# Optimization experiments

Measured on AMD Instinct MI355X. Metric: run time of the kernel, lower is better.

Reference implementation:

```python
import jax, jax.numpy as jnp
import numpy as np

T, B, NMUL = 730, 1000, 8
NEARZERO = 1e-5
LENF = 15
A_LO, A_HI = 0.1, 1.0
B_LO, B_HI = 50.0, 500.0
C_LO, C_HI = 0.0, 1.0
D_LO, D_HI = 0.01, 0.9
RA_LO, RA_HI = 0.0, 2.9
RB_LO, RB_HI = 0.0, 6.5
S_INIT, G_INIT = 50.0, 10.0


def setup_inputs() -> dict:
    key = jax.random.key(0)
    k1, k2 = jax.random.split(key)
    # forcing: prcp in [0,10) mm/day, pet in [0,5) mm/day
    x = jax.random.uniform(k1, (T, B, 2), dtype=jnp.float32) * jnp.array([10.0, 5.0], dtype=jnp.float32)
    # NN-produced raw params in [0,1): 4*NMUL physical + 2 routing
    raw_phy_static = jax.random.uniform(k2, (B, 4 * NMUL + 2), dtype=jnp.float32)
    return {"x": x, "raw_phy_static": raw_phy_static}


def _descale(p, lo, hi):
    return p * (hi - lo) + lo


def _uh_gamma(rout_a, rout_b):
    # gamma-distribution unit hydrograph, (B,) params -> (B, LENF) kernel
    aa = jax.nn.relu(rout_a)[:, None] + 0.1      # shape parameter
    theta = jax.nn.relu(rout_b)[:, None] + 0.5   # scale parameter
    t = jnp.arange(0.5, LENF, 1.0, dtype=jnp.float32)[None, :]  # midpoints 0.5..14.5
    logw = (aa - 1.0) * jnp.log(t) - t / theta - jax.scipy.special.gammaln(aa) - aa * jnp.log(theta)
    w = jnp.exp(logw)
    return w / w.sum(1, keepdims=True)


def _uh_conv(q, UH):
    # causal per-basin convolution: y[b,t] = sum_k q[b,t-k]*UH[b,k]; q (B,T), UH (B,LENF)
    n = q.shape[1]
    conv1 = lambda qb, wb: jnp.convolve(qb, wb, mode='full')[:n]
    return jax.vmap(conv1)(q, UH)


def reference(x, raw_phy_static):
    phy = raw_phy_static[:, :4 * NMUL].reshape(B, 4, NMUL)  # (B,4,NMUL)
    a = _descale(phy[:, 0], A_LO, A_HI)
    b = _descale(phy[:, 1], B_LO, B_HI)
    c = _descale(phy[:, 2], C_LO, C_HI)
    d = _descale(phy[:, 3], D_LO, D_HI)
    rout_a = _descale(raw_phy_static[:, 4 * NMUL], RA_LO, RA_HI)  # (B,)
    rout_b = _descale(raw_phy_static[:, 4 * NMUL + 1], RB_LO, RB_HI)

    ones_mul = jnp.ones((1, 1, NMUL), dtype=x.dtype)
    P = x[:, :, 0:1] * ones_mul    # (T,B,NMUL)
    PET = x[:, :, 1:2] * ones_mul  # (T,B,NMUL)

    S0 = jnp.full((B, NMUL), S_INIT, dtype=x.dtype)
    G0 = jnp.full((B, NMUL), G_INIT, dtype=x.dtype)

    def step(carry, inp):
        S, G = carry
        p, pet = inp
        W = p + S                                   # available water
        term = (W + b) / (2.0 * a)
        Y = term - jnp.sqrt(jnp.maximum(term * term - W * b / a, NEARZERO))  # ET opportunity
        S_new = Y * jnp.exp(-pet / b)               # soil storage
        AET = Y - S_new                             # actual ET
        avail = W - Y                               # water available for runoff/recharge
        Qsurf = (1.0 - c) * avail                   # direct runoff
        G_new = (G + c * avail) / (1.0 + d)         # groundwater storage
        Qgw = d * G_new                             # baseflow
        Qsim = Qsurf + Qgw
        return (S_new, G_new), (Qsim, Qsurf, Qgw, AET, S_new, G_new, W, Y)

    (_, _), (Qsim, Qsurf, Qgw, AET, Sout, Gout, Wout, Yout) = jax.lax.scan(step, (S0, G0), (P, PET))

    UH = _uh_gamma(rout_a, rout_b)                  # (B,LENF)
    Qs = _uh_conv(Qsim.mean(-1).T, UH).T[..., None]        # routed streamflow (T,B,1)
    Qsurf_r = _uh_conv(Qsurf.mean(-1).T, UH).T[..., None]  # routed surface runoff
    Qgw_r = _uh_conv(Qgw.mean(-1).T, UH).T[..., None]      # routed groundwater flow

    out = jnp.concatenate([
        Qs, Qsurf_r, Qgw_r,
        AET.mean(-1, keepdims=True),
        Sout.mean(-1, keepdims=True),
        Gout.mean(-1, keepdims=True),
    ], axis=-1)  # (T,B,6)
    return out
```

## Files before the change

kernel.cpp:

```cpp
#include <hip/hip_runtime.h>
#include <math.h>

#define T_STEPS 730
#define NB      1000
#define LENF    15
#define NEARZ   1e-5f
#define TPAD    736
#define NLANES  8000

#define STEPA(CURV, Q, SIDX)                                                   \
  {                                                                            \
    float pcp = (CURV).x, pet = (CURV).y;                                      \
    float W     = pcp + S;                                                     \
    float term  = fmaf(W, inv2a, pb2a);                                        \
    float disc  = fmaf(term, term, -(W * boa));                                \
    float r     = __builtin_amdgcn_sqrtf(fmaxf(disc, NEARZ));                  \
    float Y     = term - r;                                                    \
    float e     = __builtin_amdgcn_exp2f(pet * ninvbl2);                       \
    float Sn    = Y * e;                                                       \
    float avail = W - Y;                                                       \
    float Gn    = fmaf(pc, avail, G) * inv1pd;                                 \
    S = Sn; G = Gn;                                                            \
    sr[(Q)] = Sn;                                                              \
    gr[(Q)] = Gn;                                                              \
    if (((Q) & 3) == 3) {                                                      \
      *(float4*)(pS + (SIDX) - 3) =                                            \
          make_float4(sr[(Q) - 3], sr[(Q) - 2], sr[(Q) - 1], sr[(Q)]);         \
      *(float4*)(pG + (SIDX) - 3) =                                            \
          make_float4(gr[(Q) - 3], gr[(Q) - 2], gr[(Q) - 1], gr[(Q)]);         \
    }                                                                          \
  }

#define PREFETCH(BUF, CI)                                                      \
  _Pragma("unroll")                                                            \
  for (int j = 0; j < 8; ++j) {                                                \
      int tt = (CI) * 8 + j;                                                   \
      tt = tt < T_STEPS ? tt : (T_STEPS - 1);                                  \
      BUF[j] = xf[tt * NB + b];                                                \
  }                                                                            \
  __builtin_amdgcn_sched_barrier(0);

__global__ __launch_bounds__(64, 1) void scan_state(const float* __restrict__ x,
                                                    const float* __restrict__ raw,
                                                    float* __restrict__ snp,
                                                    float* __restrict__ gnp) {
    const int L   = threadIdx.x;
    const int gid = blockIdx.x * 64 + L;
    const int b   = gid >> 3;
    const int m   = gid & 7;

    const float* rp = raw + b * 34;
    float pa = rp[0 * 8 + m] * 0.9f + 0.1f;
    float pb = rp[1 * 8 + m] * 450.0f + 50.0f;
    float pc = rp[2 * 8 + m];
    float pd = rp[3 * 8 + m] * 0.89f + 0.01f;

    float inv2a   = 1.0f / (2.0f * pa);
    float pb2a    = pb * inv2a;
    float boa     = pb / pa;
    float ninvbl2 = -1.4426950408889634f / pb;
    float inv1pd  = 1.0f / (1.0f + pd);

    float* pS = snp + (size_t)gid * TPAD;
    float* pG = gnp + (size_t)gid * TPAD;

    float S = 50.0f, G = 10.0f;
    float sr[16], gr[16];

    const float2* __restrict__ xf = (const float2*)x;

    float2 A[8], Bb[8], Cc[8];
    PREFETCH(A, 0)
    PREFETCH(Bb, 1)

    for (int g = 0; g < 15; ++g) {
        const int c0 = 6 * g;
        PREFETCH(Cc, c0 + 2)
#pragma unroll
        for (int j = 0; j < 8; ++j) STEPA(A[j],  j,      j)
        PREFETCH(A, c0 + 3)
#pragma unroll
        for (int j = 0; j < 8; ++j) STEPA(Bb[j], 8 + j,  8 + j)
        PREFETCH(Bb, c0 + 4)
#pragma unroll
        for (int j = 0; j < 8; ++j) STEPA(Cc[j], j,      16 + j)
        PREFETCH(Cc, c0 + 5)
#pragma unroll
        for (int j = 0; j < 8; ++j) STEPA(A[j],  8 + j,  24 + j)
        PREFETCH(A, c0 + 6)
#pragma unroll
        for (int j = 0; j < 8; ++j) STEPA(Bb[j], j,      32 + j)
        PREFETCH(Bb, c0 + 7)
#pragma unroll
        for (int j = 0; j < 8; ++j) STEPA(Cc[j], 8 + j,  40 + j)
        pS += 48; pG += 48;
    }
#pragma unroll
    for (int j = 0; j < 8; ++j) STEPA(A[j], j, j)
    STEPA(Bb[0], 8, 8)
    STEPA(Bb[1], 9, 9)
    *(float2*)(pS + 8) = make_float2(sr[8], sr[9]);
    *(float2*)(pG + 8) = make_float2(gr[8], gr[9]);
}

__global__ __launch_bounds__(256) void finalize(const float* __restrict__ x,
                                                const float* __restrict__ raw,
                                                const float* __restrict__ snp,
                                                const float* __restrict__ gnp,
                                                float* __restrict__ out) {
    __shared__ float qs_sh[270], qg_sh[270];

    const int b     = blockIdx.y;
    const int tbase = blockIdx.x * 256;
    const int tid   = threadIdx.x;

    const float* rp = raw + b * 34;
    float e2s[8], omc_[8], d_[8];
#pragma unroll
    for (int m = 0; m < 8; ++m) {
        float pb = rp[8 + m] * 450.0f + 50.0f;
        e2s[m]  = 1.4426950408889634f / pb;
        omc_[m] = 1.0f - rp[16 + m];
        d_[m]   = rp[24 + m] * 0.89f + 0.01f;
    }

    const float2* __restrict__ xf = (const float2*)x;

#pragma unroll
    for (int it = 0; it < 2; ++it) {
        int idx = tid + it * 256;
        if (idx < 270) {
            int tt = tbase + idx - 14;
            float qs = 0.0f, qg = 0.0f;
            if (tt >= 0 && tt < T_STEPS) {
                float2 pc2 = xf[tt * NB + b];
                float p = pc2.x, pet = pc2.y;
                float aet = 0.0f, ssum = 0.0f, gsum = 0.0f;
                int tprev = tt > 0 ? tt - 1 : 0;
#pragma unroll
                for (int m = 0; m < 8; ++m) {
                    const float* rowS = snp + (size_t)(b * 8 + m) * TPAD;
                    const float* rowG = gnp + (size_t)(b * 8 + m) * TPAD;
                    float sn = rowS[tt];
                    float sp = tt > 0 ? rowS[tprev] : 50.0f;
                    float gn = rowG[tt];
                    float y  = sn * __builtin_amdgcn_exp2f(pet * e2s[m]);
                    float avail = (p + sp) - y;
                    qs   += omc_[m] * avail;
                    qg   += d_[m] * gn;
                    aet  += y - sn;
                    ssum += sn;
                    gsum += gn;
                }
                if (idx >= 14) {
                    float* o = out + ((size_t)tt * NB + b) * 6;
                    o[3] = aet * 0.125f;
                    o[4] = ssum * 0.125f;
                    o[5] = gsum * 0.125f;
                }
            }
            qs_sh[idx] = qs;
            qg_sh[idx] = qg;
        }
    }
    __syncthreads();

    const int t = tbase + tid;
    if (t >= T_STEPS) return;

    float ra = rp[32] * 2.9f;
    float rb = rp[33] * 6.5f;
    float aa = fmaxf(ra, 0.0f) + 0.1f;
    float th = fmaxf(rb, 0.0f) + 0.5f;
    float inv_th = 1.0f / th;
    float am1 = aa - 1.0f;
    float w[LENF];
    float sw = 0.0f;
#pragma unroll
    for (int k = 0; k < LENF; ++k) {
        float tk = (float)k + 0.5f;
        w[k] = __expf(am1 * __logf(tk) - tk * inv_th);
        sw += w[k];
    }
    float invs = 0.125f / sw;
    float ys = 0.0f, yg = 0.0f;
#pragma unroll
    for (int k = 0; k < LENF; ++k) {
        float wk = w[k] * invs;
        ys = fmaf(qs_sh[tid + 14 - k], wk, ys);
        yg = fmaf(qg_sh[tid + 14 - k], wk, yg);
    }
    float* o = out + ((size_t)t * NB + b) * 6;
    o[0] = ys + yg;
    o[1] = ys;
    o[2] = yg;
}

template <int CTRL>
__device__ __forceinline__ float dpp_mov(float x) {
    int xi = __builtin_bit_cast(int, x);
    int r  = __builtin_amdgcn_update_dpp(0, xi, CTRL, 0xF, 0xF, true);
    return __builtin_bit_cast(float, r);
}
__device__ __forceinline__ float sum8(float v) {
    v += dpp_mov<0xB1>(v);
    v += dpp_mov<0x4E>(v);
    v += dpp_mov<0x141>(v);
    return v;
}

#define STEPF(CURV)                                                            \
  {                                                                            \
    float pcp = (CURV).x, pet = (CURV).y;                                      \
    float W     = pcp + S;                                                     \
    float term  = fmaf(W, inv2a, pb2a);                                        \
    float disc  = fmaf(term, term, -(W * boa));                                \
    float r     = __builtin_amdgcn_sqrtf(fmaxf(disc, NEARZ));                  \
    float Y     = term - r;                                                    \
    float e     = __builtin_amdgcn_exp2f(pet * ninvbl2);                       \
    float Sn    = Y * e;                                                       \
    float AET   = Y - Sn;                                                      \
    float avail = W - Y;                                                       \
    float Qs    = omc * avail;                                                 \
    float Gn    = fmaf(pc, avail, G) * inv1pd;                                 \
    float Qg    = pd * Gn;                                                     \
    S = Sn; G = Gn;                                                            \
    float qs_s = sum8(Qs);                                                     \
    float qg_s = sum8(Qg);                                                     \
    float ae_s = sum8(AET);                                                    \
    float s_s  = sum8(Sn);                                                     \
    float g_s  = sum8(Gn);                                                     \
    float v = qs_s;                                                            \
    v = (m == 1) ? qg_s : v;                                                   \
    v = (m == 2) ? ae_s : v;                                                   \
    v = (m == 3) ? s_s  : v;                                                   \
    v = (m >= 4) ? g_s  : v;                                                   \
    *optr = v * 0.125f;                                                        \
    optr += incr;                                                              \
  }

__global__ __launch_bounds__(64, 1) void scan_fb(const float* __restrict__ x,
                                                 const float* __restrict__ raw,
                                                 float* __restrict__ out,
                                                 float* __restrict__ qs_ws,
                                                 float* __restrict__ qg_ws,
                                                 float* __restrict__ dummy) {
    const int L  = threadIdx.x;
    const int lb = L >> 3;
    const int m  = L & 7;
    const int b  = blockIdx.x * 8 + lb;

    const float* rp = raw + b * 34;
    float pa = rp[0 * 8 + m] * 0.9f + 0.1f;
    float pb = rp[1 * 8 + m] * 450.0f + 50.0f;
    float pc = rp[2 * 8 + m];
    float pd = rp[3 * 8 + m] * 0.89f + 0.01f;
    float inv2a   = 1.0f / (2.0f * pa);
    float pb2a    = pb * inv2a;
    float boa     = pb / pa;
    float ninvbl2 = -1.4426950408889634f / pb;
    float omc     = 1.0f - pc;
    float inv1pd  = 1.0f / (1.0f + pd);

    float* optr;
    long long incr;
    if      (m == 0) { optr = qs_ws + b;                      incr = NB;     }
    else if (m == 1) { optr = qg_ws + b;                      incr = NB;     }
    else if (m <= 4) { optr = out + (long long)b * 6 + m + 1; incr = NB * 6; }
    else             { optr = dummy + (blockIdx.x * 64 + L);  incr = 0;      }

    float S = 50.0f, G = 10.0f;
    const float2* __restrict__ xf = (const float2*)x;

    float2 A[10], B[10], C[10];
#pragma unroll
    for (int j = 0; j < 10; ++j) A[j] = xf[j * NB + b];
#pragma unroll
    for (int j = 0; j < 10; ++j) B[j] = xf[(10 + j) * NB + b];

    for (int cg = 0; cg < 24; ++cg) {
        const int c0 = 3 * cg;
#pragma unroll
        for (int j = 0; j < 10; ++j) C[j] = xf[((c0 + 2) * 10 + j) * NB + b];
        __builtin_amdgcn_sched_barrier(0);
#pragma unroll
        for (int j = 0; j < 10; ++j) STEPF(A[j]);
#pragma unroll
        for (int j = 0; j < 10; ++j) A[j] = xf[((c0 + 3) * 10 + j) * NB + b];
        __builtin_amdgcn_sched_barrier(0);
#pragma unroll
        for (int j = 0; j < 10; ++j) STEPF(B[j]);
#pragma unroll
        for (int j = 0; j < 10; ++j) {
            int t = (c0 + 4) * 10 + j;
            t = t < T_STEPS ? t : (T_STEPS - 1);
            B[j] = xf[t * NB + b];
        }
        __builtin_amdgcn_sched_barrier(0);
#pragma unroll
        for (int j = 0; j < 10; ++j) STEPF(C[j]);
    }
#pragma unroll
    for (int j = 0; j < 10; ++j) STEPF(A[j]);
}

__global__ __launch_bounds__(256) void uh_fb(const float* __restrict__ raw,
                                             float* __restrict__ uh) {
    int b = blockIdx.x * 256 + threadIdx.x;
    if (b >= NB) return;
    float ra = raw[b * 34 + 32] * 2.9f;
    float rb = raw[b * 34 + 33] * 6.5f;
    float aa = fmaxf(ra, 0.0f) + 0.1f;
    float th = fmaxf(rb, 0.0f) + 0.5f;
    float inv_th = 1.0f / th;
    float am1 = aa - 1.0f;
    float w[LENF];
    float s = 0.0f;
#pragma unroll
    for (int k = 0; k < LENF; ++k) {
        float t = (float)k + 0.5f;
        w[k] = __expf(am1 * __logf(t) - t * inv_th);
        s += w[k];
    }
    float invs = 1.0f / s;
#pragma unroll
    for (int k = 0; k < LENF; ++k) uh[k * NB + b] = w[k] * invs;
}

__global__ __launch_bounds__(256) void conv_fb(const float* __restrict__ qs_ws,
                                               const float* __restrict__ qg_ws,
                                               const float* __restrict__ uh,
                                               float* __restrict__ out) {
    int b = blockIdx.x * 256 + threadIdx.x;
    int t = blockIdx.y;
    if (b >= NB) return;
    float ys = 0.0f, yg = 0.0f;
    int kmax = t < (LENF - 1) ? t : (LENF - 1);
    for (int k = 0; k <= kmax; ++k) {
        float w = uh[k * NB + b];
        ys = fmaf(qs_ws[(t - k) * NB + b], w, ys);
        yg = fmaf(qg_ws[(t - k) * NB + b], w, yg);
    }
    float* o = out + (t * NB + b) * 6;
    o[0] = ys + yg;
    o[1] = ys;
    o[2] = yg;
}

extern "C" void kernel_launch(void* const* d_in, const int* in_sizes, int n_in,
                              void* d_out, int out_size, void* d_ws, size_t ws_size,
                              hipStream_t stream) {
    const float* x   = (const float*)d_in[0];
    const float* raw = (const float*)d_in[1];
    float* out = (float*)d_out;

    const size_t need = (size_t)NLANES * TPAD * 2 * sizeof(float);
    if (ws_size >= need) {
        float* snp = (float*)d_ws;
        float* gnp = snp + (size_t)NLANES * TPAD;
        scan_state<<<dim3(NLANES / 64), dim3(64),  0, stream>>>(x, raw, snp, gnp);
        finalize  <<<dim3(3, NB),       dim3(256), 0, stream>>>(x, raw, snp, gnp, out);
    } else {
        float* qs = (float*)d_ws;
        float* qg = qs + (size_t)T_STEPS * NB;
        float* uh = qg + (size_t)T_STEPS * NB;
        float* dm = uh + (size_t)LENF * NB;
        uh_fb  <<<dim3((NB + 255) / 256),          dim3(256), 0, stream>>>(raw, uh);
        scan_fb<<<dim3(NB / 8),                    dim3(64),  0, stream>>>(x, raw, out, qs, qg, dm);
        conv_fb<<<dim3((NB + 255) / 256, T_STEPS), dim3(256), 0, stream>>>(qs, qg, uh, out);
    }
}
```

Measured before the change: 126.7 us.

## Deepen scan prefetch to four buffers and share UH weights via LDS

The sequential scan kernel now rotates four 8-step input buffers instead of three, so loads are issued further ahead of use. Each chunk's S/G results are stored as grouped float4 writes at the start of the next chunk rather than inside the step macro. Index clamping is confined to the final prefetch. In the finalize kernel, the 15 unit-hydrograph weights are computed once per block by 15 threads and shared through LDS, instead of every thread running the log/exp per tap. This adds register pressure from the extra buffer and one more LDS read path.

```diff
diff --git a/kernel.cpp b/kernel.cpp
--- a/kernel.cpp
+++ b/kernel.cpp
@@ -8,7 +8,7 @@
 #define TPAD    736
 #define NLANES  8000
 
-#define STEPA(CURV, Q, SIDX)                                                   \
+#define STEPA(CURV, RJ)                                                        \
   {                                                                            \
     float pcp = (CURV).x, pet = (CURV).y;                                      \
     float W     = pcp + S;                                                     \
@@ -21,17 +21,16 @@
     float avail = W - Y;                                                       \
     float Gn    = fmaf(pc, avail, G) * inv1pd;                                 \
     S = Sn; G = Gn;                                                            \
-    sr[(Q)] = Sn;                                                              \
-    gr[(Q)] = Gn;                                                              \
-    if (((Q) & 3) == 3) {                                                      \
-      *(float4*)(pS + (SIDX) - 3) =                                            \
-          make_float4(sr[(Q) - 3], sr[(Q) - 2], sr[(Q) - 1], sr[(Q)]);         \
-      *(float4*)(pG + (SIDX) - 3) =                                            \
-          make_float4(gr[(Q) - 3], gr[(Q) - 2], gr[(Q) - 1], gr[(Q)]);         \
-    }                                                                          \
+    sr[(RJ)] = Sn;                                                             \
+    gr[(RJ)] = Gn;                                                             \
   }
 
-#define PREFETCH(BUF, CI)                                                      \
+#define PF(BUF, CI)                                                            \
+  _Pragma("unroll")                                                            \
+  for (int j = 0; j < 8; ++j) BUF[j] = xf[((CI) * 8 + j) * NB + b];            \
+  __builtin_amdgcn_sched_barrier(0);
+
+#define PFC(BUF, CI)                                                           \
   _Pragma("unroll")                                                            \
   for (int j = 0; j < 8; ++j) {                                                \
       int tt = (CI) * 8 + j;                                                   \
@@ -39,6 +38,18 @@
       BUF[j] = xf[tt * NB + b];                                                \
   }                                                                            \
   __builtin_amdgcn_sched_barrier(0);
+
+#define FLUSH(R)                                                               \
+  *(float4*)(pS)     = make_float4(sr[(R)], sr[(R)+1], sr[(R)+2], sr[(R)+3]);  \
+  *(float4*)(pS + 4) = make_float4(sr[(R)+4], sr[(R)+5], sr[(R)+6], sr[(R)+7]);\
+  *(float4*)(pG)     = make_float4(gr[(R)], gr[(R)+1], gr[(R)+2], gr[(R)+3]);  \
+  *(float4*)(pG + 4) = make_float4(gr[(R)+4], gr[(R)+5], gr[(R)+6], gr[(R)+7]);\
+  pS += 8; pG += 8;
+
+#define CHUNK8(RFL, BUFPF, CI, BUFC, RFILL)                                    \
+  { FLUSH(RFL) PF(BUFPF, CI) }                                                 \
+  _Pragma("unroll")                                                            \
+  for (int j = 0; j < 8; ++j) STEPA(BUFC[j], (RFILL) + j)
 
 __global__ __launch_bounds__(64, 1) void scan_state(const float* __restrict__ x,
                                                     const float* __restrict__ raw,
@@ -69,38 +80,37 @@
 
     const float2* __restrict__ xf = (const float2*)x;
 
-    float2 A[8], Bb[8], Cc[8];
-    PREFETCH(A, 0)
-    PREFETCH(Bb, 1)
-
-    for (int g = 0; g < 15; ++g) {
-        const int c0 = 6 * g;
-        PREFETCH(Cc, c0 + 2)
-#pragma unroll
-        for (int j = 0; j < 8; ++j) STEPA(A[j],  j,      j)
-        PREFETCH(A, c0 + 3)
-#pragma unroll
-        for (int j = 0; j < 8; ++j) STEPA(Bb[j], 8 + j,  8 + j)
-        PREFETCH(Bb, c0 + 4)
-#pragma unroll
-        for (int j = 0; j < 8; ++j) STEPA(Cc[j], j,      16 + j)
-        PREFETCH(Cc, c0 + 5)
-#pragma unroll
-        for (int j = 0; j < 8; ++j) STEPA(A[j],  8 + j,  24 + j)
-        PREFETCH(A, c0 + 6)
-#pragma unroll
-        for (int j = 0; j < 8; ++j) STEPA(Bb[j], j,      32 + j)
-        PREFETCH(Bb, c0 + 7)
-#pragma unroll
-        for (int j = 0; j < 8; ++j) STEPA(Cc[j], 8 + j,  40 + j)
-        pS += 48; pG += 48;
-    }
-#pragma unroll
-    for (int j = 0; j < 8; ++j) STEPA(A[j], j, j)
-    STEPA(Bb[0], 8, 8)
-    STEPA(Bb[1], 9, 9)
-    *(float2*)(pS + 8) = make_float2(sr[8], sr[9]);
-    *(float2*)(pG + 8) = make_float2(gr[8], gr[9]);
+    float2 A[8], B[8], C[8], D[8];
+    PF(A, 0) PF(B, 1) PF(C, 2)
+
+    { PF(D, 3) }
+#pragma unroll
+    for (int j = 0; j < 8; ++j) STEPA(A[j], j);
+
+    for (int g = 0; g < 21; ++g) {
+        const int c0 = 4 * g + 1;
+        CHUNK8(0, A, c0 + 3, B, 8);
+        CHUNK8(8, B, c0 + 4, C, 0);
+        CHUNK8(0, C, c0 + 5, D, 8);
+        CHUNK8(8, D, c0 + 6, A, 0);
+    }
+    CHUNK8(0, A, 88, B, 8);
+    CHUNK8(8, B, 89, C, 0);
+    CHUNK8(0, C, 90, D, 8);
+    { FLUSH(8) PFC(D, 91) }
+#pragma unroll
+    for (int j = 0; j < 8; ++j) STEPA(A[j], j);
+    { FLUSH(0) }
+#pragma unroll
+    for (int j = 0; j < 8; ++j) STEPA(B[j], 8 + j);
+    { FLUSH(8) }
+#pragma unroll
+    for (int j = 0; j < 8; ++j) STEPA(C[j], j);
+    STEPA(D[0], 8)
+    STEPA(D[1], 9)
+    { FLUSH(0) }
+    *(float2*)(pS) = make_float2(sr[8], sr[9]);
+    *(float2*)(pG) = make_float2(gr[8], gr[9]);
 }
 
 __global__ __launch_bounds__(256) void finalize(const float* __restrict__ x,
@@ -108,13 +118,23 @@
                                                 const float* __restrict__ snp,
                                                 const float* __restrict__ gnp,
                                                 float* __restrict__ out) {
-    __shared__ float qs_sh[270], qg_sh[270];
+    __shared__ float qs_sh[270], qg_sh[270], w_sh[16];
 
     const int b     = blockIdx.y;
     const int tbase = blockIdx.x * 256;
     const int tid   = threadIdx.x;
 
     const float* rp = raw + b * 34;
+
+    if (tid < LENF) {
+        float ra = rp[32] * 2.9f;
+        float rb = rp[33] * 6.5f;
+        float aa = fmaxf(ra, 0.0f) + 0.1f;
+        float th = fmaxf(rb, 0.0f) + 0.5f;
+        float tk = (float)tid + 0.5f;
+        w_sh[tid] = __expf((aa - 1.0f) * __logf(tk) - tk / th);
+    }
+
     float e2s[8], omc_[8], d_[8];
 #pragma unroll
     for (int m = 0; m < 8; ++m) {
@@ -168,25 +188,14 @@
     const int t = tbase + tid;
     if (t >= T_STEPS) return;
 
-    float ra = rp[32] * 2.9f;
-    float rb = rp[33] * 6.5f;
-    float aa = fmaxf(ra, 0.0f) + 0.1f;
-    float th = fmaxf(rb, 0.0f) + 0.5f;
-    float inv_th = 1.0f / th;
-    float am1 = aa - 1.0f;
-    float w[LENF];
     float sw = 0.0f;
 #pragma unroll
-    for (int k = 0; k < LENF; ++k) {
-        float tk = (float)k + 0.5f;
-        w[k] = __expf(am1 * __logf(tk) - tk * inv_th);
-        sw += w[k];
-    }
+    for (int k = 0; k < LENF; ++k) sw += w_sh[k];
     float invs = 0.125f / sw;
     float ys = 0.0f, yg = 0.0f;
 #pragma unroll
     for (int k = 0; k < LENF; ++k) {
-        float wk = w[k] * invs;
+        float wk = w_sh[k] * invs;
         ys = fmaf(qs_sh[tid + 14 - k], wk, ys);
         yg = fmaf(qg_sh[tid + 14 - k], wk, yg);
     }
```

Result: no change. 127.6 us (+0.7%).
